# Performance work log

Measured on AMD Instinct MI355X. Metric: run time of the kernel, lower is better.

Reference implementation:

```python
import jax, jax.numpy as jnp
import numpy as np

N = 16384   # 32 graphs x 512 nodes
E_RAND = 500000
H, C, D, F, L = 4, 64, 256, 1024, 4  # heads, head_dim, model dim, ffn dim, layers


def setup_inputs() -> dict:
    key = jax.random.key(0)
    ks = jax.random.split(key, 8)
    ei = jax.random.randint(ks[0], (2, E_RAND), 0, N)
    loops = jnp.arange(N)
    edge_index = jnp.concatenate([ei, jnp.stack([loops, loops])], axis=1)  # add_self_loops
    s = 0.05
    return dict(
        hf=jax.random.normal(ks[1], (N, D), dtype=jnp.float32),
        hs=jax.random.normal(ks[2], (N, D), dtype=jnp.float32),
        edge_index=edge_index,
        Wgat=jax.random.normal(ks[3], (2, L, D, D), dtype=jnp.float32) * s,
        att_src=jax.random.normal(ks[4], (2, L, H, C), dtype=jnp.float32) * s,
        att_dst=jax.random.normal(ks[5], (2, L, H, C), dtype=jnp.float32) * s,
        bias_gat=jnp.zeros((2, L, D), dtype=jnp.float32),
        W1=jax.random.normal(ks[6], (2, L, D, F), dtype=jnp.float32) * s,
        b1=jnp.zeros((2, L, F), dtype=jnp.float32),
        W2=jax.random.normal(ks[7], (2, L, F, D), dtype=jnp.float32) * s,
        b2=jnp.zeros((2, L, D), dtype=jnp.float32),
        g1=jnp.ones((2, L, D), dtype=jnp.float32),
        bt1=jnp.zeros((2, L, D), dtype=jnp.float32),
        g2=jnp.ones((2, L, D), dtype=jnp.float32),
        bt2=jnp.zeros((2, L, D), dtype=jnp.float32),
    )


def _ln(x, g, b):
    m = jnp.mean(x, -1, keepdims=True)
    v = jnp.var(x, -1, keepdims=True)
    return (x - m) * jax.lax.rsqrt(v + 1e-5) * g + b


def _gat_encoder_layer(x, src, dst, Wg, asr, ads, bg, W1, b1, W2, b2, g1, bt1, g2, bt2):
    # GATConv (PyG semantics): linear proj, per-edge attention, segment softmax over dst
    h = (x @ Wg).reshape(N, H, C)                       # [N,H,C]
    a_s = (h * asr).sum(-1)                             # [N,H]
    a_d = (h * ads).sum(-1)                             # [N,H]
    e = jax.nn.leaky_relu(a_s[src] + a_d[dst], 0.2)     # [E,H]
    m = jax.ops.segment_max(e, dst, num_segments=N)
    ex = jnp.exp(e - m[dst])
    den = jax.ops.segment_sum(ex, dst, num_segments=N)
    alpha = ex / jnp.maximum(den[dst], 1e-16)           # [E,H]
    agg = jax.ops.segment_sum(h[src] * alpha[:, :, None], dst, num_segments=N)
    out = agg.reshape(N, H * C) + bg                    # concat heads + bias
    # residual + norm1 (dropout=0.0)
    x1 = _ln(out + x, g1, bt1)
    # FFN + residual + norm2
    f = jax.nn.relu(x1 @ W1 + b1) @ W2 + b2
    return _ln(f + x1, g2, bt2)


def reference(hf, hs, edge_index, Wgat, att_src, att_dst, bias_gat, W1, b1, W2, b2, g1, bt1, g2, bt2):
    src, dst = edge_index[0], edge_index[1]
    for i in range(L):
        hf_new = _gat_encoder_layer(hf + hs, src, dst, Wgat[0, i], att_src[0, i], att_dst[0, i],
                                    bias_gat[0, i], W1[0, i], b1[0, i], W2[0, i], b2[0, i],
                                    g1[0, i], bt1[0, i], g2[0, i], bt2[0, i])
        hs = _gat_encoder_layer(hs, src, dst, Wgat[1, i], att_src[1, i], att_dst[1, i],
                                bias_gat[1, i], W1[1, i], b1[1, i], W2[1, i], b2[1, i],
                                g1[1, i], bt1[1, i], g2[1, i], bt2[1, i])
        hf = hf_new
    return (hf, hs)
```

## Files before the change

kernel.cpp:

```cpp
#include <hip/hip_runtime.h>

#define Nn 16384
#define Dm 256
#define Ff 1024

typedef __attribute__((ext_vector_type(8))) short bf16x8;
typedef __attribute__((ext_vector_type(4))) float f32x4;

typedef const __attribute__((address_space(1))) unsigned int glb_u32;
typedef __attribute__((address_space(3))) unsigned int lds_u32;

__device__ __forceinline__ void async_copy16(const void* g, void* l) {
  __builtin_amdgcn_global_load_lds((glb_u32*)g, (lds_u32*)l, 16, 0, 0);
}

__device__ __forceinline__ unsigned short f2bf(float f) {
  union { float f; unsigned u; } v; v.f = f;
  return (unsigned short)((v.u + 0x7FFFu + ((v.u >> 16) & 1u)) >> 16);
}

__device__ __forceinline__ float bf2f(unsigned short u) {
  union { unsigned u; float f; } v; v.u = ((unsigned)u) << 16;
  return v.f;
}

__device__ __forceinline__ float sel4(float4 v, int h) {
  float r = v.x;
  r = (h == 1) ? v.y : r;
  r = (h == 2) ? v.z : r;
  r = (h == 3) ? v.w : r;
  return r;
}

__global__ __launch_bounds__(256) void wconvt_kernel(const float* __restrict__ w,
                                                     unsigned short* __restrict__ wt,
                                                     int K, int J) {
  __shared__ unsigned short t[64][65];
  int b = blockIdx.z;
  int j0 = blockIdx.x * 64, k0 = blockIdx.y * 64;
  int tj = threadIdx.x & 63, q = threadIdx.x >> 6;
  const float* wb = w + (size_t)b * K * J;
#pragma unroll
  for (int r = 0; r < 16; ++r) {
    int k = r * 4 + q;
    t[k][tj] = f2bf(wb[(size_t)(k0 + k) * J + j0 + tj]);
  }
  __syncthreads();
  unsigned short* wtb = wt + (size_t)b * K * J;
#pragma unroll
  for (int r = 0; r < 16; ++r) {
    int j = r * 4 + q;
    wtb[(size_t)(j0 + j) * K + k0 + tj] = t[tj][j];
  }
}

__global__ void count_kernel(const int* __restrict__ dst, int E, int* __restrict__ cnt) {
  for (int e = blockIdx.x * blockDim.x + threadIdx.x; e < E; e += gridDim.x * blockDim.x)
    atomicAdd(&cnt[dst[e]], 1);
}

__global__ __launch_bounds__(256) void scan1_kernel(const int* __restrict__ cnt,
                                                    int* __restrict__ part,
                                                    int* __restrict__ bsum) {
  __shared__ int sd[256];
  int b = blockIdx.x, tid = threadIdx.x;
  int v = cnt[b * 256 + tid];
  sd[tid] = v;
  __syncthreads();
  for (int offt = 1; offt < 256; offt <<= 1) {
    int t = (tid >= offt) ? sd[tid - offt] : 0;
    __syncthreads();
    sd[tid] += t;
    __syncthreads();
  }
  part[b * 256 + tid] = sd[tid] - v;
  if (tid == 255) bsum[b] = sd[255];
}

__global__ __launch_bounds__(64) void scan2_kernel(const int* __restrict__ bsum,
                                                   int* __restrict__ bbase,
                                                   int* __restrict__ rowptr) {
  __shared__ int sd[64];
  int tid = threadIdx.x;
  int v = bsum[tid];
  sd[tid] = v;
  __syncthreads();
  for (int offt = 1; offt < 64; offt <<= 1) {
    int t = (tid >= offt) ? sd[tid - offt] : 0;
    __syncthreads();
    sd[tid] += t;
    __syncthreads();
  }
  bbase[tid] = sd[tid] - v;
  if (tid == 63) rowptr[Nn] = sd[63];
}

__global__ __launch_bounds__(256) void scan3_kernel(const int* __restrict__ part,
                                                    const int* __restrict__ bbase,
                                                    int* __restrict__ rowptr,
                                                    int* __restrict__ cursor) {
  int b = blockIdx.x, tid = threadIdx.x;
  int v = part[b * 256 + tid] + bbase[b];
  rowptr[b * 256 + tid] = v;
  cursor[b * 256 + tid] = v;
}

__global__ void fill_kernel(const int* __restrict__ src, const int* __restrict__ dst, int E,
                            int* __restrict__ cursor, int* __restrict__ csrc) {
  for (int e = blockIdx.x * blockDim.x + threadIdx.x; e < E; e += gridDim.x * blockDim.x) {
    int pos = atomicAdd(&cursor[dst[e]], 1);
    csrc[pos] = src[e];
  }
}

__global__ void prep_kernel(const float* __restrict__ hf, const float* __restrict__ hs,
                            unsigned short* __restrict__ x01b, int total) {
  const size_t ZS = (size_t)Nn * Dm;
  for (int i = blockIdx.x * blockDim.x + threadIdx.x; i < total; i += gridDim.x * blockDim.x) {
    float a = hf[i], b = hs[i];
    x01b[i] = f2bf(a + b);
    x01b[ZS + i] = f2bf(b);
  }
}

__global__ __launch_bounds__(256, 2) void proj_kernel(
    const unsigned short* __restrict__ xib, const unsigned short* __restrict__ Wgt_l,
    unsigned short* __restrict__ hbuf2, const float* __restrict__ asr_l,
    const float* __restrict__ ads_l, float* __restrict__ a_s2, float* __restrict__ a_d2) {
  __shared__ __align__(16) unsigned short sA[128 * 64];
  __shared__ __align__(16) unsigned short sB[64 * 64];
  const int K = 256;
  const size_t ZS = (size_t)Nn * Dm;
  int tid = threadIdx.x;
  int wave = tid >> 6, lane = tid & 63;
  int l16 = lane & 15, lhi = lane >> 4;
  int brow = blockIdx.x, bcol = blockIdx.y, z = blockIdx.z;
  int wm = wave >> 1, wn = wave & 1;

  const unsigned short* Ab = xib + z * ZS + (size_t)brow * 128 * K;
  const unsigned short* Bb = Wgt_l + (size_t)z * 4 * 65536 + (size_t)bcol * 64 * K;
  int lrow = lane >> 3, lk = (lane & 7) * 8;

  f32x4 acc[4][2] = {};

  for (int k0 = 0; k0 < K; k0 += 64) {
#pragma unroll
    for (int r = 0; r < 4; ++r) {
      int rb = r * 32 + wave * 8;
      async_copy16(Ab + (size_t)(rb + lrow) * K + k0 + lk, &sA[rb * 64]);
      if (r < 2)
        async_copy16(Bb + (size_t)(rb + lrow) * K + k0 + lk, &sB[rb * 64]);
    }
    __syncthreads();
#pragma unroll
    for (int kk = 0; kk < 2; ++kk) {
      bf16x8 af[4], bfr[2];
#pragma unroll
      for (int mi = 0; mi < 4; ++mi)
        af[mi] = *(const bf16x8*)&sA[(wm * 64 + mi * 16 + l16) * 64 + kk * 32 + lhi * 8];
#pragma unroll
      for (int ni = 0; ni < 2; ++ni)
        bfr[ni] = *(const bf16x8*)&sB[(wn * 32 + ni * 16 + l16) * 64 + kk * 32 + lhi * 8];
#pragma unroll
      for (int mi = 0; mi < 4; ++mi)
#pragma unroll
        for (int ni = 0; ni < 2; ++ni)
          acc[mi][ni] = __builtin_amdgcn_mfma_f32_16x16x32_bf16(af[mi], bfr[ni], acc[mi][ni], 0, 0, 0);
    }
    __syncthreads();
  }

  unsigned short* hb = hbuf2 + z * ZS;
  const float* asr_p = asr_l + z * 1024 + bcol * 64;
  const float* ads_p = ads_l + z * 1024 + bcol * 64;
  float as0 = asr_p[wn * 32 + l16],      ad0 = ads_p[wn * 32 + l16];
  float as1 = asr_p[wn * 32 + 16 + l16], ad1 = ads_p[wn * 32 + 16 + l16];
  float* sredS = (float*)sA;
  float* sredD = (float*)sA + 256;

#pragma unroll
  for (int mi = 0; mi < 4; ++mi) {
#pragma unroll
    for (int j = 0; j < 4; ++j) {
      int r = brow * 128 + wm * 64 + mi * 16 + lhi * 4 + j;
      float v0 = acc[mi][0][j], v1 = acc[mi][1][j];
      hb[(size_t)r * 256 + bcol * 64 + wn * 32 + l16] = f2bf(v0);
      hb[(size_t)r * 256 + bcol * 64 + wn * 32 + 16 + l16] = f2bf(v1);
      float ps = v0 * as0 + v1 * as1;
      float pd = v0 * ad0 + v1 * ad1;
#pragma unroll
      for (int off = 1; off < 16; off <<= 1) {
        ps += __shfl_xor(ps, off);
        pd += __shfl_xor(pd, off);
      }
      if (l16 == 0) {
        int rl = mi * 16 + lhi * 4 + j;
        sredS[wm * 128 + wn * 64 + rl] = ps;
        sredD[wm * 128 + wn * 64 + rl] = pd;
      }
    }
  }
  __syncthreads();
  if (tid < 128) {
    int w = tid >> 6, rl = tid & 63;
    float s = sredS[w * 128 + rl] + sredS[w * 128 + 64 + rl];
    float d = sredD[w * 128 + rl] + sredD[w * 128 + 64 + rl];
    int row = brow * 128 + tid;
    a_s2[(size_t)z * Nn * 4 + row * 4 + bcol] = s;
    a_d2[(size_t)z * Nn * 4 + row * 4 + bcol] = d;
  }
}

__global__ __launch_bounds__(256, 2) void ffn1_kernel(
    const unsigned short* __restrict__ A2, const unsigned short* __restrict__ Bt_l,
    unsigned short* __restrict__ out2, const float* __restrict__ b1_l) {
  const int K = 256, Ncol = Ff;
  const size_t ZS = (size_t)Nn * Dm;
  __shared__ __align__(16) unsigned short sA[128 * 64];
  __shared__ __align__(16) unsigned short sB[128 * 64];
  int tid = threadIdx.x, wave = tid >> 6, lane = tid & 63;
  int l16 = lane & 15, lhi = lane >> 4;
  int brow = blockIdx.x, bcol = blockIdx.y, z = blockIdx.z;
  int wm = wave >> 1, wn = wave & 1;

  const unsigned short* Ab = A2 + z * ZS + (size_t)brow * 128 * K;
  const unsigned short* Bb = Bt_l + (size_t)z * 4 * Ff * 256 + (size_t)bcol * 128 * K;
  int lrow = lane >> 3, lk = (lane & 7) * 8;

  f32x4 acc[4][4] = {};

  for (int k0 = 0; k0 < K; k0 += 64) {
#pragma unroll
    for (int r = 0; r < 4; ++r) {
      int rb = r * 32 + wave * 8;
      async_copy16(Ab + (size_t)(rb + lrow) * K + k0 + lk, &sA[rb * 64]);
      async_copy16(Bb + (size_t)(rb + lrow) * K + k0 + lk, &sB[rb * 64]);
    }
    __syncthreads();
#pragma unroll
    for (int kk = 0; kk < 2; ++kk) {
      bf16x8 af[4], bfr[4];
#pragma unroll
      for (int mi = 0; mi < 4; ++mi)
        af[mi] = *(const bf16x8*)&sA[(wm * 64 + mi * 16 + l16) * 64 + kk * 32 + lhi * 8];
#pragma unroll
      for (int ni = 0; ni < 4; ++ni)
        bfr[ni] = *(const bf16x8*)&sB[(wn * 64 + ni * 16 + l16) * 64 + kk * 32 + lhi * 8];
#pragma unroll
      for (int mi = 0; mi < 4; ++mi)
#pragma unroll
        for (int ni = 0; ni < 4; ++ni)
          acc[mi][ni] = __builtin_amdgcn_mfma_f32_16x16x32_bf16(af[mi], bfr[ni], acc[mi][ni], 0, 0, 0);
    }
    __syncthreads();
  }

  unsigned short* outB = out2 + (size_t)z * Nn * Ff;
  const float* bias = b1_l + z * 4096;
#pragma unroll
  for (int mi = 0; mi < 4; ++mi) {
#pragma unroll
    for (int ni = 0; ni < 4; ++ni) {
#pragma unroll
      for (int j = 0; j < 4; ++j) {
        int r = brow * 128 + wm * 64 + mi * 16 + lhi * 4 + j;
        int c = bcol * 128 + wn * 64 + ni * 16 + l16;
        float v = acc[mi][ni][j] + bias[c];
        v = v > 0.f ? v : 0.f;
        outB[(size_t)r * Ncol + c] = f2bf(v);
      }
    }
  }
}

__global__ __launch_bounds__(256, 2) void ffn2_kernel(
    const unsigned short* __restrict__ A2, const unsigned short* __restrict__ Bt_l,
    unsigned short* __restrict__ out2, const float* __restrict__ b2_l,
    const unsigned short* __restrict__ resid2) {
  const int K = Ff, Ncol = 256;
  const size_t ZS = (size_t)Nn * Dm;
  __shared__ __align__(16) unsigned short sA[128 * 64];
  __shared__ __align__(16) unsigned short sB[64 * 64];
  int tid = threadIdx.x, wave = tid >> 6, lane = tid & 63;
  int l16 = lane & 15, lhi = lane >> 4;
  int brow = blockIdx.x, bcol = blockIdx.y, z = blockIdx.z;
  int wm = wave >> 1, wn = wave & 1;

  const unsigned short* Ab = A2 + (size_t)z * Nn * Ff + (size_t)brow * 128 * K;
  const unsigned short* Bb = Bt_l + (size_t)z * 4 * Ff * 256 + (size_t)bcol * 64 * K;
  int lrow = lane >> 3, lk = (lane & 7) * 8;

  f32x4 acc[4][2] = {};

  for (int k0 = 0; k0 < K; k0 += 64) {
#pragma unroll
    for (int r = 0; r < 4; ++r) {
      int rb = r * 32 + wave * 8;
      async_copy16(Ab + (size_t)(rb + lrow) * K + k0 + lk, &sA[rb * 64]);
      if (r < 2)
        async_copy16(Bb + (size_t)(rb + lrow) * K + k0 + lk, &sB[rb * 64]);
    }
    __syncthreads();
#pragma unroll
    for (int kk = 0; kk < 2; ++kk) {
      bf16x8 af[4], bfr[2];
#pragma unroll
      for (int mi = 0; mi < 4; ++mi)
        af[mi] = *(const bf16x8*)&sA[(wm * 64 + mi * 16 + l16) * 64 + kk * 32 + lhi * 8];
#pragma unroll
      for (int ni = 0; ni < 2; ++ni)
        bfr[ni] = *(const bf16x8*)&sB[(wn * 32 + ni * 16 + l16) * 64 + kk * 32 + lhi * 8];
#pragma unroll
      for (int mi = 0; mi < 4; ++mi)
#pragma unroll
        for (int ni = 0; ni < 2; ++ni)
          acc[mi][ni] = __builtin_amdgcn_mfma_f32_16x16x32_bf16(af[mi], bfr[ni], acc[mi][ni], 0, 0, 0);
    }
    __syncthreads();
  }

  unsigned short* outB = out2 + z * ZS;
  const float* bias = b2_l + z * 1024;
  const unsigned short* resid = resid2 + z * ZS;
#pragma unroll
  for (int mi = 0; mi < 4; ++mi) {
#pragma unroll
    for (int ni = 0; ni < 2; ++ni) {
#pragma unroll
      for (int j = 0; j < 4; ++j) {
        int r = brow * 128 + wm * 64 + mi * 16 + lhi * 4 + j;
        int c = bcol * 64 + wn * 32 + ni * 16 + l16;
        float v = acc[mi][ni][j] + bias[c] + bf2f(resid[(size_t)r * Ncol + c]);
        outB[(size_t)r * Ncol + c] = f2bf(v);
      }
    }
  }
}

__global__ __launch_bounds__(256) void agg_kernel(
    const unsigned short* __restrict__ hbuf2, const float* __restrict__ a_s2,
    const float* __restrict__ a_d2,
    const int* __restrict__ rowptr, const int* __restrict__ csrc,
    const float* __restrict__ bias_l, const unsigned short* __restrict__ x01b,
    const float* __restrict__ g1_l, const float* __restrict__ bt1_l,
    unsigned short* __restrict__ x1b2) {
  __shared__ float sw[4][320];
  __shared__ int ssrc[4][64];
  const size_t ZS = (size_t)Nn * Dm;
  int z = blockIdx.y;
  const unsigned short* hb = hbuf2 + z * ZS;
  const float* a_s = a_s2 + (size_t)z * Nn * 4;
  const float* a_d = a_d2 + (size_t)z * Nn * 4;
  const float* bias = bias_l + z * 1024;
  const unsigned short* xres = x01b + z * ZS;
  const float* g1 = g1_l + z * 1024;
  const float* bt1 = bt1_l + z * 1024;
  unsigned short* x1b = x1b2 + z * ZS;

  int wave = threadIdx.x >> 6, lane = threadIdx.x & 63;
  int n = blockIdx.x * 4 + wave;
  int l32 = lane & 31;
  int par = lane >> 5;
  int hch = l32 >> 3;
  int c0 = l32 * 8;
  int beg = rowptr[n], end = rowptr[n + 1];
  float4 adv = *(const float4*)&a_d[n * 4];
  const float NI = -__builtin_inff();
  float4 m4 = {NI, NI, NI, NI};
  float acc[8] = {};
  float den = 0.f;

  for (int base = beg; base < end; base += 64) {
    int cnt = min(64, end - base);
    float4 ev = {NI, NI, NI, NI};
    if (lane < cnt) {
      int s = csrc[base + lane];
      ssrc[wave][lane] = s;
      float4 as = *(const float4*)&a_s[s * 4];
      float e0 = as.x + adv.x; ev.x = e0 > 0.f ? e0 : 0.2f * e0;
      float e1 = as.y + adv.y; ev.y = e1 > 0.f ? e1 : 0.2f * e1;
      float e2 = as.z + adv.z; ev.z = e2 > 0.f ? e2 : 0.2f * e2;
      float e3 = as.w + adv.w; ev.w = e3 > 0.f ? e3 : 0.2f * e3;
    }
    float4 mv = ev;
#pragma unroll
    for (int off = 32; off; off >>= 1) {
      mv.x = fmaxf(mv.x, __shfl_xor(mv.x, off));
      mv.y = fmaxf(mv.y, __shfl_xor(mv.y, off));
      mv.z = fmaxf(mv.z, __shfl_xor(mv.z, off));
      mv.w = fmaxf(mv.w, __shfl_xor(mv.w, off));
    }
    float4 m4n;
    m4n.x = fmaxf(m4.x, mv.x); m4n.y = fmaxf(m4.y, mv.y);
    m4n.z = fmaxf(m4.z, mv.z); m4n.w = fmaxf(m4.w, mv.w);
    float rm = __expf(sel4(m4, hch) - sel4(m4n, hch));
#pragma unroll
    for (int j = 0; j < 8; ++j) acc[j] *= rm;
    den *= rm;
    if (lane < cnt) {
      float* swl = &sw[wave][lane * 5];
      swl[0] = __expf(ev.x - m4n.x);
      swl[1] = __expf(ev.y - m4n.y);
      swl[2] = __expf(ev.z - m4n.z);
      swl[3] = __expf(ev.w - m4n.w);
    }
    m4 = m4n;
    __builtin_amdgcn_wave_barrier();
    for (int i = par; i < cnt; i += 2) {
      float w = sw[wave][i * 5 + hch];
      int s_i = ssrc[wave][i];
      bf16x8 hv = *(const bf16x8*)(hb + (size_t)s_i * 256 + c0);
#pragma unroll
      for (int j = 0; j < 8; ++j)
        acc[j] = fmaf(bf2f((unsigned short)hv[j]), w, acc[j]);
      den += w;
    }
    __builtin_amdgcn_wave_barrier();
  }

#pragma unroll
  for (int j = 0; j < 8; ++j) acc[j] += __shfl_xor(acc[j], 32);
  den += __shfl_xor(den, 32);

  float invden = 1.f / fmaxf(den, 1e-16f);
  bf16x8 rv = *(const bf16x8*)(xres + (size_t)n * 256 + c0);
  float outv[8];
  float s1 = 0.f, s2 = 0.f;
#pragma unroll
  for (int j = 0; j < 8; ++j) {
    float v = acc[j] * invden + bias[c0 + j] + bf2f((unsigned short)rv[j]);
    outv[j] = v;
    s1 += v;
    s2 += v * v;
  }
#pragma unroll
  for (int off = 16; off; off >>= 1) {
    s1 += __shfl_xor(s1, off);
    s2 += __shfl_xor(s2, off);
  }
  float mean = s1 * (1.f / 256.f);
  float var = s2 * (1.f / 256.f) - mean * mean;
  float rst = rsqrtf(var + 1e-5f);
  if (par == 0) {
    unsigned short yb[8];
#pragma unroll
    for (int j = 0; j < 8; ++j)
      yb[j] = f2bf((outv[j] - mean) * rst * g1[c0 + j] + bt1[c0 + j]);
    *(bf16x8*)&x1b[(size_t)n * 256 + c0] = *(bf16x8*)yb;
  }
}

template <int PREP>
__global__ __launch_bounds__(256) void ln2_kernel(const unsigned short* __restrict__ tb2,
                                                  const float* __restrict__ g2_l,
                                                  const float* __restrict__ bt2_l,
                                                  float* __restrict__ out_hf,
                                                  float* __restrict__ out_hs,
                                                  unsigned short* __restrict__ x01b) {
  const size_t ZS = (size_t)Nn * Dm;
  int wave = threadIdx.x >> 6, lane = threadIdx.x & 63;
  int n = blockIdx.x * 4 + wave;
  int c0 = lane * 4;
  size_t idx = (size_t)n * 256 + c0;
  ushort4 u0 = *(const ushort4*)&tb2[idx];
  ushort4 u1 = *(const ushort4*)&tb2[ZS + idx];
  float v0[4] = {bf2f(u0.x), bf2f(u0.y), bf2f(u0.z), bf2f(u0.w)};
  float v1[4] = {bf2f(u1.x), bf2f(u1.y), bf2f(u1.z), bf2f(u1.w)};
  float a0 = 0.f, b0 = 0.f, a1 = 0.f, b1 = 0.f;
#pragma unroll
  for (int j = 0; j < 4; ++j) {
    a0 += v0[j]; b0 += v0[j] * v0[j];
    a1 += v1[j]; b1 += v1[j] * v1[j];
  }
#pragma unroll
  for (int off = 32; off; off >>= 1) {
    a0 += __shfl_xor(a0, off);
    b0 += __shfl_xor(b0, off);
    a1 += __shfl_xor(a1, off);
    b1 += __shfl_xor(b1, off);
  }
  float m0 = a0 * (1.f / 256.f), m1 = a1 * (1.f / 256.f);
  float r0 = rsqrtf(b0 * (1.f / 256.f) - m0 * m0 + 1e-5f);
  float r1 = rsqrtf(b1 * (1.f / 256.f) - m1 * m1 + 1e-5f);
  float4 y0, y1;
  unsigned short p0[4], p1[4];
#pragma unroll
  for (int j = 0; j < 4; ++j) {
    float yf = (v0[j] - m0) * r0 * g2_l[c0 + j] + bt2_l[c0 + j];
    float ys = (v1[j] - m1) * r1 * g2_l[1024 + c0 + j] + bt2_l[1024 + c0 + j];
    ((float*)&y0)[j] = yf;
    ((float*)&y1)[j] = ys;
    if (PREP) { p0[j] = f2bf(yf + ys); p1[j] = f2bf(ys); }
  }
  *(float4*)&out_hf[idx] = y0;
  *(float4*)&out_hs[idx] = y1;
  if (PREP) {
    *(ushort4*)&x01b[idx] = *(ushort4*)p0;
    *(ushort4*)&x01b[ZS + idx] = *(ushort4*)p1;
  }
}

extern "C" void kernel_launch(void* const* d_in, const int* in_sizes, int n_in,
                              void* d_out, int out_size, void* d_ws, size_t ws_size,
                              hipStream_t stream) {
  const float* hf_in = (const float*)d_in[0];
  const float* hs_in = (const float*)d_in[1];
  const int* ei = (const int*)d_in[2];
  const int E = in_sizes[2] / 2;
  const float* Wgat = (const float*)d_in[3];
  const float* att_src = (const float*)d_in[4];
  const float* att_dst = (const float*)d_in[5];
  const float* bias_gat = (const float*)d_in[6];
  const float* W1 = (const float*)d_in[7];
  const float* b1 = (const float*)d_in[8];
  const float* W2 = (const float*)d_in[9];
  const float* b2 = (const float*)d_in[10];
  const float* g1 = (const float*)d_in[11];
  const float* bt1 = (const float*)d_in[12];
  const float* g2 = (const float*)d_in[13];
  const float* bt2 = (const float*)d_in[14];
  const int* src = ei;
  const int* dst = ei + E;
  const size_t ZS = (size_t)Nn * Dm;

  char* wsp = (char*)d_ws;
  size_t off = 0;
  auto carve = [&](size_t bytes) -> void* {
    void* p = wsp + off;
    off += (bytes + 255) & ~(size_t)255;
    return p;
  };
  unsigned short* Wgt  = (unsigned short*)carve((size_t)8 * 256 * 256 * 2);
  unsigned short* W1t  = (unsigned short*)carve((size_t)8 * 256 * 1024 * 2);
  unsigned short* W2t  = (unsigned short*)carve((size_t)8 * 1024 * 256 * 2);
  int* cnt      = (int*)carve((size_t)Nn * 4);
  int* rowptr   = (int*)carve((size_t)(Nn + 1) * 4);
  int* cursor   = (int*)carve((size_t)Nn * 4);
  int* part     = (int*)carve((size_t)Nn * 4);
  int* bsum     = (int*)carve((size_t)64 * 4);
  int* bbase    = (int*)carve((size_t)64 * 4);
  int* csrc     = (int*)carve((size_t)E * 4);
  unsigned short* x01b = (unsigned short*)carve(2 * ZS * 2);
  unsigned short* hbuf2 = (unsigned short*)carve(2 * ZS * 2);
  float* a_s2   = (float*)carve((size_t)2 * Nn * 4 * 4);
  float* a_d2   = (float*)carve((size_t)2 * Nn * 4 * 4);
  unsigned short* x1b2 = (unsigned short*)carve(2 * ZS * 2);
  unsigned short* tb2  = (unsigned short*)carve(2 * ZS * 2);
  unsigned short* f_b2 = (unsigned short*)carve((size_t)2 * Nn * Ff * 2);
  if (off > ws_size) return;

  wconvt_kernel<<<dim3(4, 4, 8), 256, 0, stream>>>(Wgat, Wgt, 256, 256);
  wconvt_kernel<<<dim3(16, 4, 8), 256, 0, stream>>>(W1, W1t, 256, 1024);
  wconvt_kernel<<<dim3(4, 16, 8), 256, 0, stream>>>(W2, W2t, 1024, 256);
  hipMemsetAsync(cnt, 0, (size_t)Nn * 4, stream);
  count_kernel<<<1024, 256, 0, stream>>>(dst, E, cnt);
  scan1_kernel<<<64, 256, 0, stream>>>(cnt, part, bsum);
  scan2_kernel<<<1, 64, 0, stream>>>(bsum, bbase, rowptr);
  scan3_kernel<<<64, 256, 0, stream>>>(part, bbase, rowptr, cursor);
  fill_kernel<<<1024, 256, 0, stream>>>(src, dst, E, cursor, csrc);

  float* out_hf = (float*)d_out;
  float* out_hs = out_hf + ZS;

  prep_kernel<<<2048, 256, 0, stream>>>(hf_in, hs_in, x01b, Nn * Dm);

  for (int l = 0; l < 4; ++l) {
    proj_kernel<<<dim3(128, 4, 2), 256, 0, stream>>>(
        x01b, Wgt + (size_t)l * 65536, hbuf2,
        att_src + l * 256, att_dst + l * 256, a_s2, a_d2);
    agg_kernel<<<dim3(Nn / 4, 2), 256, 0, stream>>>(
        hbuf2, a_s2, a_d2, rowptr, csrc,
        bias_gat + l * 256, x01b, g1 + l * 256, bt1 + l * 256, x1b2);
    ffn1_kernel<<<dim3(128, 8, 2), 256, 0, stream>>>(
        x1b2, W1t + (size_t)l * 256 * 1024, f_b2, b1 + l * 1024);
    ffn2_kernel<<<dim3(128, 4, 2), 256, 0, stream>>>(
        f_b2, W2t + (size_t)l * 1024 * 256, tb2, b2 + l * 256, x1b2);
    if (l < 3) {
      ln2_kernel<1><<<Nn / 4, 256, 0, stream>>>(tb2, g2 + l * 256, bt2 + l * 256,
                                                out_hf, out_hs, x01b);
    } else {
      ln2_kernel<0><<<Nn / 4, 256, 0, stream>>>(tb2, g2 + l * 256, bt2 + l * 256,
                                                out_hf, out_hs, x01b);
    }
  }
}
```

Measured before the change: 659.0 us.

## Interleave both streams' projections per node and aggregate both in one agg pass

The projection output and attention logits for the two streams (hf and hs) are now stored interleaved per node, so each node's row holds both streams. The aggregation kernel processes both streams in a single launch, sharing the CSR index reads and the softmax setup, and loads the two half-rows together. It also adds a single-pass fast path for nodes with at most 64 neighbours that skips the online-softmax rescaling. The cost is higher register pressure, a larger shared buffer, and half as many blocks in the aggregation launch.

```diff
diff --git a/kernel.cpp b/kernel.cpp
--- a/kernel.cpp
+++ b/kernel.cpp
@@ -29,6 +29,16 @@
   r = (h == 1) ? v.y : r;
   r = (h == 2) ? v.z : r;
   r = (h == 3) ? v.w : r;
+  return r;
+}
+
+__device__ __forceinline__ float4 lrelu4(float4 a, float4 b) {
+  float4 r;
+  float e;
+  e = a.x + b.x; r.x = e > 0.f ? e : 0.2f * e;
+  e = a.y + b.y; r.y = e > 0.f ? e : 0.2f * e;
+  e = a.z + b.z; r.z = e > 0.f ? e : 0.2f * e;
+  e = a.w + b.w; r.w = e > 0.f ? e : 0.2f * e;
   return r;
 }
 
@@ -125,8 +135,8 @@
 
 __global__ __launch_bounds__(256, 2) void proj_kernel(
     const unsigned short* __restrict__ xib, const unsigned short* __restrict__ Wgt_l,
-    unsigned short* __restrict__ hbuf2, const float* __restrict__ asr_l,
-    const float* __restrict__ ads_l, float* __restrict__ a_s2, float* __restrict__ a_d2) {
+    unsigned short* __restrict__ hbI, const float* __restrict__ asr_l,
+    const float* __restrict__ ads_l, float* __restrict__ a_sI, float* __restrict__ a_dI) {
   __shared__ __align__(16) unsigned short sA[128 * 64];
   __shared__ __align__(16) unsigned short sB[64 * 64];
   const int K = 256;
@@ -170,7 +180,6 @@
     __syncthreads();
   }
 
-  unsigned short* hb = hbuf2 + z * ZS;
   const float* asr_p = asr_l + z * 1024 + bcol * 64;
   const float* ads_p = ads_l + z * 1024 + bcol * 64;
   float as0 = asr_p[wn * 32 + l16],      ad0 = ads_p[wn * 32 + l16];
@@ -184,8 +193,9 @@
     for (int j = 0; j < 4; ++j) {
       int r = brow * 128 + wm * 64 + mi * 16 + lhi * 4 + j;
       float v0 = acc[mi][0][j], v1 = acc[mi][1][j];
-      hb[(size_t)r * 256 + bcol * 64 + wn * 32 + l16] = f2bf(v0);
-      hb[(size_t)r * 256 + bcol * 64 + wn * 32 + 16 + l16] = f2bf(v1);
+      size_t rb = (size_t)r * 512 + z * 256 + bcol * 64 + wn * 32;
+      hbI[rb + l16] = f2bf(v0);
+      hbI[rb + 16 + l16] = f2bf(v1);
       float ps = v0 * as0 + v1 * as1;
       float pd = v0 * ad0 + v1 * ad1;
 #pragma unroll
@@ -206,8 +216,8 @@
     float s = sredS[w * 128 + rl] + sredS[w * 128 + 64 + rl];
     float d = sredD[w * 128 + rl] + sredD[w * 128 + 64 + rl];
     int row = brow * 128 + tid;
-    a_s2[(size_t)z * Nn * 4 + row * 4 + bcol] = s;
-    a_d2[(size_t)z * Nn * 4 + row * 4 + bcol] = d;
+    a_sI[(size_t)row * 8 + z * 4 + bcol] = s;
+    a_dI[(size_t)row * 8 + z * 4 + bcol] = d;
   }
 }
 
@@ -338,24 +348,15 @@
 }
 
 __global__ __launch_bounds__(256) void agg_kernel(
-    const unsigned short* __restrict__ hbuf2, const float* __restrict__ a_s2,
-    const float* __restrict__ a_d2,
+    const unsigned short* __restrict__ hbI, const float* __restrict__ a_sI,
+    const float* __restrict__ a_dI,
     const int* __restrict__ rowptr, const int* __restrict__ csrc,
     const float* __restrict__ bias_l, const unsigned short* __restrict__ x01b,
     const float* __restrict__ g1_l, const float* __restrict__ bt1_l,
     unsigned short* __restrict__ x1b2) {
-  __shared__ float sw[4][320];
+  __shared__ float sw[4][576];
   __shared__ int ssrc[4][64];
   const size_t ZS = (size_t)Nn * Dm;
-  int z = blockIdx.y;
-  const unsigned short* hb = hbuf2 + z * ZS;
-  const float* a_s = a_s2 + (size_t)z * Nn * 4;
-  const float* a_d = a_d2 + (size_t)z * Nn * 4;
-  const float* bias = bias_l + z * 1024;
-  const unsigned short* xres = x01b + z * ZS;
-  const float* g1 = g1_l + z * 1024;
-  const float* bt1 = bt1_l + z * 1024;
-  unsigned short* x1b = x1b2 + z * ZS;
 
   int wave = threadIdx.x >> 6, lane = threadIdx.x & 63;
   int n = blockIdx.x * 4 + wave;
@@ -364,89 +365,165 @@
   int hch = l32 >> 3;
   int c0 = l32 * 8;
   int beg = rowptr[n], end = rowptr[n + 1];
-  float4 adv = *(const float4*)&a_d[n * 4];
+  float4 adv0 = *(const float4*)&a_dI[n * 8];
+  float4 adv1 = *(const float4*)&a_dI[n * 8 + 4];
   const float NI = -__builtin_inff();
-  float4 m4 = {NI, NI, NI, NI};
-  float acc[8] = {};
-  float den = 0.f;
-
-  for (int base = beg; base < end; base += 64) {
-    int cnt = min(64, end - base);
-    float4 ev = {NI, NI, NI, NI};
+  float acc0[8] = {}, acc1[8] = {};
+  float den0 = 0.f, den1 = 0.f;
+
+  if (end - beg <= 64) {
+    int cnt = end - beg;
+    float4 ev0 = {NI, NI, NI, NI}, ev1 = {NI, NI, NI, NI};
     if (lane < cnt) {
-      int s = csrc[base + lane];
+      int s = csrc[beg + lane];
       ssrc[wave][lane] = s;
-      float4 as = *(const float4*)&a_s[s * 4];
-      float e0 = as.x + adv.x; ev.x = e0 > 0.f ? e0 : 0.2f * e0;
-      float e1 = as.y + adv.y; ev.y = e1 > 0.f ? e1 : 0.2f * e1;
-      float e2 = as.z + adv.z; ev.z = e2 > 0.f ? e2 : 0.2f * e2;
-      float e3 = as.w + adv.w; ev.w = e3 > 0.f ? e3 : 0.2f * e3;
-    }
-    float4 mv = ev;
+      ev0 = lrelu4(*(const float4*)&a_sI[s * 8], adv0);
+      ev1 = lrelu4(*(const float4*)&a_sI[s * 8 + 4], adv1);
+    }
+    float4 mv0 = ev0, mv1 = ev1;
 #pragma unroll
     for (int off = 32; off; off >>= 1) {
-      mv.x = fmaxf(mv.x, __shfl_xor(mv.x, off));
-      mv.y = fmaxf(mv.y, __shfl_xor(mv.y, off));
-      mv.z = fmaxf(mv.z, __shfl_xor(mv.z, off));
-      mv.w = fmaxf(mv.w, __shfl_xor(mv.w, off));
-    }
-    float4 m4n;
-    m4n.x = fmaxf(m4.x, mv.x); m4n.y = fmaxf(m4.y, mv.y);
-    m4n.z = fmaxf(m4.z, mv.z); m4n.w = fmaxf(m4.w, mv.w);
-    float rm = __expf(sel4(m4, hch) - sel4(m4n, hch));
-#pragma unroll
-    for (int j = 0; j < 8; ++j) acc[j] *= rm;
-    den *= rm;
+      mv0.x = fmaxf(mv0.x, __shfl_xor(mv0.x, off));
+      mv0.y = fmaxf(mv0.y, __shfl_xor(mv0.y, off));
+      mv0.z = fmaxf(mv0.z, __shfl_xor(mv0.z, off));
+      mv0.w = fmaxf(mv0.w, __shfl_xor(mv0.w, off));
+      mv1.x = fmaxf(mv1.x, __shfl_xor(mv1.x, off));
+      mv1.y = fmaxf(mv1.y, __shfl_xor(mv1.y, off));
+      mv1.z = fmaxf(mv1.z, __shfl_xor(mv1.z, off));
+      mv1.w = fmaxf(mv1.w, __shfl_xor(mv1.w, off));
+    }
     if (lane < cnt) {
-      float* swl = &sw[wave][lane * 5];
-      swl[0] = __expf(ev.x - m4n.x);
-      swl[1] = __expf(ev.y - m4n.y);
-      swl[2] = __expf(ev.z - m4n.z);
-      swl[3] = __expf(ev.w - m4n.w);
-    }
-    m4 = m4n;
+      float* swl = &sw[wave][lane * 9];
+      swl[0] = __expf(ev0.x - mv0.x); swl[1] = __expf(ev0.y - mv0.y);
+      swl[2] = __expf(ev0.z - mv0.z); swl[3] = __expf(ev0.w - mv0.w);
+      swl[4] = __expf(ev1.x - mv1.x); swl[5] = __expf(ev1.y - mv1.y);
+      swl[6] = __expf(ev1.z - mv1.z); swl[7] = __expf(ev1.w - mv1.w);
+    }
     __builtin_amdgcn_wave_barrier();
     for (int i = par; i < cnt; i += 2) {
-      float w = sw[wave][i * 5 + hch];
       int s_i = ssrc[wave][i];
-      bf16x8 hv = *(const bf16x8*)(hb + (size_t)s_i * 256 + c0);
+      float w0 = sw[wave][i * 9 + hch];
+      float w1 = sw[wave][i * 9 + 4 + hch];
+      const unsigned short* rowp = hbI + (size_t)s_i * 512 + c0;
+      bf16x8 h0 = *(const bf16x8*)rowp;
+      bf16x8 h1 = *(const bf16x8*)(rowp + 256);
 #pragma unroll
       for (int j = 0; j < 8; ++j)
-        acc[j] = fmaf(bf2f((unsigned short)hv[j]), w, acc[j]);
-      den += w;
-    }
-    __builtin_amdgcn_wave_barrier();
-  }
-
-#pragma unroll
-  for (int j = 0; j < 8; ++j) acc[j] += __shfl_xor(acc[j], 32);
-  den += __shfl_xor(den, 32);
-
-  float invden = 1.f / fmaxf(den, 1e-16f);
-  bf16x8 rv = *(const bf16x8*)(xres + (size_t)n * 256 + c0);
-  float outv[8];
-  float s1 = 0.f, s2 = 0.f;
+        acc0[j] = fmaf(bf2f((unsigned short)h0[j]), w0, acc0[j]);
+#pragma unroll
+      for (int j = 0; j < 8; ++j)
+        acc1[j] = fmaf(bf2f((unsigned short)h1[j]), w1, acc1[j]);
+      den0 += w0;
+      den1 += w1;
+    }
+  } else {
+    float4 m40 = {NI, NI, NI, NI}, m41 = {NI, NI, NI, NI};
+    for (int base = beg; base < end; base += 64) {
+      int cnt = min(64, end - base);
+      float4 ev0 = {NI, NI, NI, NI}, ev1 = {NI, NI, NI, NI};
+      if (lane < cnt) {
+        int s = csrc[base + lane];
+        ssrc[wave][lane] = s;
+        ev0 = lrelu4(*(const float4*)&a_sI[s * 8], adv0);
+        ev1 = lrelu4(*(const float4*)&a_sI[s * 8 + 4], adv1);
+      }
+      float4 mv0 = ev0, mv1 = ev1;
+#pragma unroll
+      for (int off = 32; off; off >>= 1) {
+        mv0.x = fmaxf(mv0.x, __shfl_xor(mv0.x, off));
+        mv0.y = fmaxf(mv0.y, __shfl_xor(mv0.y, off));
+        mv0.z = fmaxf(mv0.z, __shfl_xor(mv0.z, off));
+        mv0.w = fmaxf(mv0.w, __shfl_xor(mv0.w, off));
+        mv1.x = fmaxf(mv1.x, __shfl_xor(mv1.x, off));
+        mv1.y = fmaxf(mv1.y, __shfl_xor(mv1.y, off));
+        mv1.z = fmaxf(mv1.z, __shfl_xor(mv1.z, off));
+        mv1.w = fmaxf(mv1.w, __shfl_xor(mv1.w, off));
+      }
+      float4 m40n, m41n;
+      m40n.x = fmaxf(m40.x, mv0.x); m40n.y = fmaxf(m40.y, mv0.y);
+      m40n.z = fmaxf(m40.z, mv0.z); m40n.w = fmaxf(m40.w, mv0.w);
+      m41n.x = fmaxf(m41.x, mv1.x); m41n.y = fmaxf(m41.y, mv1.y);
+      m41n.z = fmaxf(m41.z, mv1.z); m41n.w = fmaxf(m41.w, mv1.w);
+      float rm0 = __expf(sel4(m40, hch) - sel4(m40n, hch));
+      float rm1 = __expf(sel4(m41, hch) - sel4(m41n, hch));
+#pragma unroll
+      for (int j = 0; j < 8; ++j) { acc0[j] *= rm0; acc1[j] *= rm1; }
+      den0 *= rm0;
+      den1 *= rm1;
+      if (lane < cnt) {
+        float* swl = &sw[wave][lane * 9];
+        swl[0] = __expf(ev0.x - m40n.x); swl[1] = __expf(ev0.y - m40n.y);
+        swl[2] = __expf(ev0.z - m40n.z); swl[3] = __expf(ev0.w - m40n.w);
+        swl[4] = __expf(ev1.x - m41n.x); swl[5] = __expf(ev1.y - m41n.y);
+        swl[6] = __expf(ev1.z - m41n.z); swl[7] = __expf(ev1.w - m41n.w);
+      }
+      m40 = m40n;
+      m41 = m41n;
+      __builtin_amdgcn_wave_barrier();
+      for (int i = par; i < cnt; i += 2) {
+        int s_i = ssrc[wave][i];
+        float w0 = sw[wave][i * 9 + hch];
+        float w1 = sw[wave][i * 9 + 4 + hch];
+        const unsigned short* rowp = hbI + (size_t)s_i * 512 + c0;
+        bf16x8 h0 = *(const bf16x8*)rowp;
+        bf16x8 h1 = *(const bf16x8*)(rowp + 256);
+#pragma unroll
+        for (int j = 0; j < 8; ++j)
+          acc0[j] = fmaf(bf2f((unsigned short)h0[j]), w0, acc0[j]);
+#pragma unroll
+        for (int j = 0; j < 8; ++j)
+          acc1[j] = fmaf(bf2f((unsigned short)h1[j]), w1, acc1[j]);
+        den0 += w0;
+        den1 += w1;
+      }
+      __builtin_amdgcn_wave_barrier();
+    }
+  }
+
 #pragma unroll
   for (int j = 0; j < 8; ++j) {
-    float v = acc[j] * invden + bias[c0 + j] + bf2f((unsigned short)rv[j]);
-    outv[j] = v;
-    s1 += v;
-    s2 += v * v;
+    acc0[j] += __shfl_xor(acc0[j], 32);
+    acc1[j] += __shfl_xor(acc1[j], 32);
+  }
+  den0 += __shfl_xor(den0, 32);
+  den1 += __shfl_xor(den1, 32);
+
+  float invden0 = 1.f / fmaxf(den0, 1e-16f);
+  float invden1 = 1.f / fmaxf(den1, 1e-16f);
+  bf16x8 rv0 = *(const bf16x8*)(x01b + (size_t)n * 256 + c0);
+  bf16x8 rv1 = *(const bf16x8*)(x01b + ZS + (size_t)n * 256 + c0);
+  float outv0[8], outv1[8];
+  float s10 = 0.f, s20 = 0.f, s11 = 0.f, s21 = 0.f;
+#pragma unroll
+  for (int j = 0; j < 8; ++j) {
+    float v0 = acc0[j] * invden0 + bias_l[c0 + j] + bf2f((unsigned short)rv0[j]);
+    float v1 = acc1[j] * invden1 + bias_l[1024 + c0 + j] + bf2f((unsigned short)rv1[j]);
+    outv0[j] = v0; outv1[j] = v1;
+    s10 += v0; s20 += v0 * v0;
+    s11 += v1; s21 += v1 * v1;
   }
 #pragma unroll
   for (int off = 16; off; off >>= 1) {
-    s1 += __shfl_xor(s1, off);
-    s2 += __shfl_xor(s2, off);
-  }
-  float mean = s1 * (1.f / 256.f);
-  float var = s2 * (1.f / 256.f) - mean * mean;
-  float rst = rsqrtf(var + 1e-5f);
+    s10 += __shfl_xor(s10, off);
+    s20 += __shfl_xor(s20, off);
+    s11 += __shfl_xor(s11, off);
+    s21 += __shfl_xor(s21, off);
+  }
+  float mean0 = s10 * (1.f / 256.f);
+  float var0 = s20 * (1.f / 256.f) - mean0 * mean0;
+  float rst0 = rsqrtf(var0 + 1e-5f);
+  float mean1 = s11 * (1.f / 256.f);
+  float var1 = s21 * (1.f / 256.f) - mean1 * mean1;
+  float rst1 = rsqrtf(var1 + 1e-5f);
   if (par == 0) {
-    unsigned short yb[8];
-#pragma unroll
-    for (int j = 0; j < 8; ++j)
-      yb[j] = f2bf((outv[j] - mean) * rst * g1[c0 + j] + bt1[c0 + j]);
-    *(bf16x8*)&x1b[(size_t)n * 256 + c0] = *(bf16x8*)yb;
+    unsigned short yb0[8], yb1[8];
+#pragma unroll
+    for (int j = 0; j < 8; ++j) {
+      yb0[j] = f2bf((outv0[j] - mean0) * rst0 * g1_l[c0 + j] + bt1_l[c0 + j]);
+      yb1[j] = f2bf((outv1[j] - mean1) * rst1 * g1_l[1024 + c0 + j] + bt1_l[1024 + c0 + j]);
+    }
+    *(bf16x8*)&x1b2[(size_t)n * 256 + c0] = *(bf16x8*)yb0;
+    *(bf16x8*)&x1b2[ZS + (size_t)n * 256 + c0] = *(bf16x8*)yb1;
   }
 }
 
@@ -541,9 +618,9 @@
   int* bbase    = (int*)carve((size_t)64 * 4);
   int* csrc     = (int*)carve((size_t)E * 4);
   unsigned short* x01b = (unsigned short*)carve(2 * ZS * 2);
-  unsigned short* hbuf2 = (unsigned short*)carve(2 * ZS * 2);
-  float* a_s2   = (float*)carve((size_t)2 * Nn * 4 * 4);
-  float* a_d2   = (float*)carve((size_t)2 * Nn * 4 * 4);
+  unsigned short* hbI  = (unsigned short*)carve(2 * ZS * 2);
+  float* a_sI   = (float*)carve((size_t)Nn * 8 * 4);
+  float* a_dI   = (float*)carve((size_t)Nn * 8 * 4);
   unsigned short* x1b2 = (unsigned short*)carve(2 * ZS * 2);
   unsigned short* tb2  = (unsigned short*)carve(2 * ZS * 2);
   unsigned short* f_b2 = (unsigned short*)carve((size_t)2 * Nn * Ff * 2);
@@ -566,10 +643,10 @@
 
   for (int l = 0; l < 4; ++l) {
     proj_kernel<<<dim3(128, 4, 2), 256, 0, stream>>>(
-        x01b, Wgt + (size_t)l * 65536, hbuf2,
-        att_src + l * 256, att_dst + l * 256, a_s2, a_d2);
-    agg_kernel<<<dim3(Nn / 4, 2), 256, 0, stream>>>(
-        hbuf2, a_s2, a_d2, rowptr, csrc,
+        x01b, Wgt + (size_t)l * 65536, hbI,
+        att_src + l * 256, att_dst + l * 256, a_sI, a_dI);
+    agg_kernel<<<Nn / 4, 256, 0, stream>>>(
+        hbI, a_sI, a_dI, rowptr, csrc,
         bias_gat + l * 256, x01b, g1 + l * 256, bt1 + l * 256, x1b2);
     ffn1_kernel<<<dim3(128, 8, 2), 256, 0, stream>>>(
         x1b2, W1t + (size_t)l * 256 * 1024, f_b2, b1 + l * 1024);
```

Measured after the change: 708.6 us. 7.5% more time.
